# Kernel tuning notes

Measured on AMD Instinct MI355X. Metric: run time of the kernel, lower is better.

## Reference

```python
import math
import jax, jax.numpy as jnp
import numpy as np

B, S, D = 4, 2048, 1280
H, HD = 16, 80  # num_heads, head_dim
LOG2E = 1.442695041


def setup_inputs() -> dict:
    key = jax.random.key(0)
    ks = jax.random.split(key, 6)
    hidden_states = jax.random.normal(ks[0], (B, S, D), dtype=jnp.float32)
    # additive causal mask: 0 on/below diagonal, large negative above
    causal = jnp.tril(jnp.ones((S, S), dtype=bool))
    attention_mask = jnp.where(causal, 0.0, -1e9).astype(jnp.float32)[None, None, :, :]
    attention_mask = jnp.broadcast_to(attention_mask, (B, 1, S, S))
    scaling = jax.random.normal(ks[1], (HD,), dtype=jnp.float32)
    fan = 1.0 / math.sqrt(D)
    qkv_w = jax.random.normal(ks[2], (3 * H * HD, D), dtype=jnp.float32) * fan
    qkv_b = jax.random.normal(ks[3], (3 * H * HD,), dtype=jnp.float32) * fan
    o_w = jax.random.normal(ks[4], (D, H * HD), dtype=jnp.float32) * (1.0 / math.sqrt(H * HD))
    o_b = jax.random.normal(ks[5], (D,), dtype=jnp.float32) * fan
    return {
        "hidden_states": hidden_states,
        "attention_mask": attention_mask,
        "scaling": scaling,
        "qkv_w": qkv_w,
        "qkv_b": qkv_b,
        "o_w": o_w,
        "o_b": o_b,
    }


def reference(hidden_states, attention_mask, scaling, qkv_w, qkv_b, o_w, o_b):
    b, s, _ = hidden_states.shape
    qkv = hidden_states @ qkv_w.T + qkv_b  # [b, s, 3*H*HD]
    xq, xk, xv = jnp.split(qkv, [H * HD, 2 * H * HD], axis=-1)
    xq = xq.reshape(b, s, H, HD)
    xk = xk.reshape(b, s, H, HD)
    xv = xv.reshape(b, s, H, HD)
    # per-dim query scaling: softplus(scaling) * log2(e) / sqrt(head_dim)
    scale = jax.nn.softplus(scaling) * (LOG2E / math.sqrt(HD))
    xq = xq * scale[None, None, None, :]
    scores = jnp.einsum("bqhd,bkhd->bhqk", xq, xk) + attention_mask  # [b,H,s,s]
    probs = jax.nn.softmax(scores.astype(jnp.float32), axis=-1).astype(xq.dtype)
    out = jnp.einsum("bhqk,bkhd->bqhd", probs, xv).reshape(b, s, H * HD)
    return out @ o_w.T + o_b
```

## Files before the change

### kernel.cpp

```cpp
#include <hip/hip_runtime.h>
#include <math.h>

#define B_ 4
#define S_ 2048
#define D_ 1280
#define H_ 16
#define HD_ 80
#define HHD (H_ * HD_)
#define QKVN (3 * H_ * HD_)

typedef __bf16 bf16x8 __attribute__((ext_vector_type(8)));
typedef float  f32x4  __attribute__((ext_vector_type(4)));

__global__ __launch_bounds__(256) void cvt_bf16(
    const float* __restrict__ in, __bf16* __restrict__ out, int n8)
{
    const int i = blockIdx.x * 256 + threadIdx.x;
    if (i < n8) {
        const float4 a = ((const float4*)in)[2 * (size_t)i];
        const float4 b = ((const float4*)in)[2 * (size_t)i + 1];
        bf16x8 v = {(__bf16)a.x, (__bf16)a.y, (__bf16)a.z, (__bf16)a.w,
                    (__bf16)b.x, (__bf16)b.y, (__bf16)b.z, (__bf16)b.w};
        *(bf16x8*)(out + 8 * (size_t)i) = v;
    }
}

__device__ __forceinline__ void async_copy16(const void* g, void* l)
{
    __builtin_amdgcn_global_load_lds(
        (const __attribute__((address_space(1))) unsigned int*)g,
        (__attribute__((address_space(3))) unsigned int*)l, 16, 0, 0);
}

__device__ __forceinline__ void stage128x64(
    const __bf16* __restrict__ src, int K, char* lds, int tid)
{
    const int wave = tid >> 6, lane = tid & 63;
#pragma unroll
    for (int i = 0; i < 4; ++i) {
        const int c = (wave * 4 + i) * 64 + lane;
        const int r = c >> 3;
        const int g = (c & 7) ^ (r & 7);
        async_copy16(src + (size_t)r * K + g * 8, lds + (wave * 4 + i) * 1024);
    }
}

__device__ __forceinline__ bf16x8 frag_ld(const char* lds, int m, int j)
{
    return *(const bf16x8*)(lds + m * 128 + ((j ^ (m & 7)) << 4));
}

__device__ __forceinline__ void mfma_loop(
    const __bf16* __restrict__ A, const __bf16* __restrict__ W, int K,
    char* ldsA, char* ldsB, int tid, f32x4 acc[4][4])
{
    const int wave = tid >> 6;
    const int wm = wave >> 1, wn = wave & 1;
    const int l16 = tid & 15, quad = (tid & 63) >> 4;

#pragma unroll
    for (int mi = 0; mi < 4; ++mi)
#pragma unroll
        for (int ni = 0; ni < 4; ++ni) acc[mi][ni] = (f32x4){0.f, 0.f, 0.f, 0.f};

    for (int k0 = 0; k0 < K; k0 += 64) {
        __syncthreads();
        stage128x64(A + k0, K, ldsA, tid);
        stage128x64(W + k0, K, ldsB, tid);
        __syncthreads();
#pragma unroll
        for (int ks = 0; ks < 2; ++ks) {
            bf16x8 af[4], bfr[4];
#pragma unroll
            for (int mi = 0; mi < 4; ++mi)
                af[mi] = frag_ld(ldsA, wm * 64 + mi * 16 + l16, ks * 4 + quad);
#pragma unroll
            for (int ni = 0; ni < 4; ++ni)
                bfr[ni] = frag_ld(ldsB, wn * 64 + ni * 16 + l16, ks * 4 + quad);
#pragma unroll
            for (int mi = 0; mi < 4; ++mi)
#pragma unroll
                for (int ni = 0; ni < 4; ++ni)
                    acc[mi][ni] = __builtin_amdgcn_mfma_f32_16x16x32_bf16(
                        af[mi], bfr[ni], acc[mi][ni], 0, 0, 0);
        }
    }
}

__global__ __launch_bounds__(256) void gemm_qkv_mfma(
    const __bf16* __restrict__ Ab, const __bf16* __restrict__ Wb,
    const float* __restrict__ bias, const float* __restrict__ scaling,
    __bf16* __restrict__ Qb, __bf16* __restrict__ Kb, __bf16* __restrict__ Vtb)
{
    __shared__ __align__(16) char ldsA[128 * 128];
    __shared__ __align__(16) char ldsB[128 * 128];
    const int tid = threadIdx.x;
    const int m0 = blockIdx.y * 128, n0 = blockIdx.x * 128;

    f32x4 acc[4][4];
    mfma_loop(Ab + (size_t)m0 * D_, Wb + (size_t)n0 * D_, D_, ldsA, ldsB, tid, acc);

    const int wave = tid >> 6, wm = wave >> 1, wn = wave & 1;
    const int l16 = tid & 15, quad = (tid & 63) >> 4;
    const int sec = n0 / HHD;

#pragma unroll
    for (int ni = 0; ni < 4; ++ni) {
        const int col = n0 + wn * 64 + ni * 16 + l16;
        const int cis = col - sec * HHD;
        const int h = cis / HD_;
        const int d = cis - h * HD_;
        const float bv = bias[col];
        float qsv = 0.f;
        if (sec == 0)
            qsv = log1pf(expf(scaling[d])) * (1.442695041f / 8.944271910f);
#pragma unroll
        for (int mi = 0; mi < 4; ++mi) {
#pragma unroll
            for (int r = 0; r < 4; ++r) {
                const int row = m0 + wm * 64 + mi * 16 + quad * 4 + r;
                const int bb = row >> 11;
                const int s = row & (S_ - 1);
                const size_t bh = (size_t)(bb * H_ + h);
                const float v = acc[mi][ni][r] + bv;
                if (sec == 0)      Qb[(bh * S_ + s) * HD_ + d] = (__bf16)(v * qsv);
                else if (sec == 1) Kb[(bh * S_ + s) * HD_ + d] = (__bf16)v;
                else               Vtb[(bh * HD_ + d) * S_ + s] = (__bf16)v;
            }
        }
    }
}

__global__ __launch_bounds__(256) void gemm_o_mfma(
    const __bf16* __restrict__ Ab, const __bf16* __restrict__ Wb,
    const float* __restrict__ bias, float* __restrict__ C)
{
    __shared__ __align__(16) char ldsA[128 * 128];
    __shared__ __align__(16) char ldsB[128 * 128];
    const int tid = threadIdx.x;
    const int m0 = blockIdx.y * 128, n0 = blockIdx.x * 128;

    f32x4 acc[4][4];
    mfma_loop(Ab + (size_t)m0 * D_, Wb + (size_t)n0 * D_, D_, ldsA, ldsB, tid, acc);

    const int wave = tid >> 6, wm = wave >> 1, wn = wave & 1;
    const int l16 = tid & 15, quad = (tid & 63) >> 4;

#pragma unroll
    for (int ni = 0; ni < 4; ++ni) {
        const int col = n0 + wn * 64 + ni * 16 + l16;
        const float bv = bias[col];
#pragma unroll
        for (int mi = 0; mi < 4; ++mi) {
#pragma unroll
            for (int r = 0; r < 4; ++r) {
                const int row = m0 + wm * 64 + mi * 16 + quad * 4 + r;
                C[(size_t)row * D_ + col] = acc[mi][ni][r] + bv;
            }
        }
    }
}

template<int CTRL>
__device__ __forceinline__ float dppmov(float v)
{
    return __builtin_bit_cast(float,
        __builtin_amdgcn_update_dpp(0, __builtin_bit_cast(int, v),
                                    CTRL, 0xf, 0xf, true));
}
__device__ __forceinline__ float rmax16(float v)
{
    v = fmaxf(v, dppmov<0xB1>(v));
    v = fmaxf(v, dppmov<0x4E>(v));
    v = fmaxf(v, dppmov<0x141>(v));
    v = fmaxf(v, dppmov<0x140>(v));
    return v;
}
__device__ __forceinline__ float rsum16(float v)
{
    v += dppmov<0xB1>(v);
    v += dppmov<0x4E>(v);
    v += dppmov<0x141>(v);
    v += dppmov<0x140>(v);
    return v;
}

__global__ __launch_bounds__(256, 4) void attn_v5(
    const __bf16* __restrict__ Qb, const __bf16* __restrict__ Kb,
    const __bf16* __restrict__ Vtb, __bf16* __restrict__ out)
{
    __shared__ __align__(16) __bf16 Ps[4][2][16][40];

    const int tid = threadIdx.x;
    const int wave = tid >> 6;
    const int lane = tid & 63;
    const int l16 = lane & 15;
    const int quad = lane >> 4;
    const int b = blockIdx.z, h = blockIdx.y;
    const int bh = b * H_ + h;
    const int x = blockIdx.x;
    const int q_lo = 64 * x + 16 * wave;
    const int q_hi = 64 * (31 - x) + 16 * wave;

    const __bf16* Kbase = Kb + (size_t)bh * S_ * HD_;
    const __bf16* Vbase = Vtb + (size_t)bh * HD_ * S_;

    bf16x8 qfL[3], qfH[3];
    {
        const __bf16* QrowL = Qb + ((size_t)bh * S_ + q_lo + l16) * HD_;
        const __bf16* QrowH = Qb + ((size_t)bh * S_ + q_hi + l16) * HD_;
        qfL[0] = *(const bf16x8*)(QrowL + quad * 8);
        qfL[1] = *(const bf16x8*)(QrowL + 32 + quad * 8);
        qfH[0] = *(const bf16x8*)(QrowH + quad * 8);
        qfH[1] = *(const bf16x8*)(QrowH + 32 + quad * 8);
        bf16x8 zL = {}, zH = {};
        if (quad < 2) {
            zL = *(const bf16x8*)(QrowL + 64 + quad * 8);
            zH = *(const bf16x8*)(QrowH + 64 + quad * 8);
        }
        qfL[2] = zL; qfH[2] = zH;
    }

    float mL[4], lL[4], mH[4], lH[4];
#pragma unroll
    for (int i = 0; i < 4; ++i) { mL[i] = -1e30f; lL[i] = 0.f; mH[i] = -1e30f; lH[i] = 0.f; }
    f32x4 oL[5], oH[5];
#pragma unroll
    for (int t = 0; t < 5; ++t) { oL[t] = (f32x4){0.f,0.f,0.f,0.f}; oH[t] = (f32x4){0.f,0.f,0.f,0.f}; }

    const int nkt_lo = (q_lo + 16 + 31) >> 5;
    const int nkt_hi = (q_hi + 16 + 31) >> 5;

    for (int kt = 0; kt < nkt_hi; ++kt) {
        const int k0 = kt * 32;
        const bool do_lo = (kt < nkt_lo);

        f32x4 sL[2], sH[2];
#pragma unroll
        for (int t = 0; t < 2; ++t) {
            const __bf16* Krow = Kbase + (size_t)(k0 + t * 16 + l16) * HD_;
            const bf16x8 kf0 = *(const bf16x8*)(Krow + quad * 8);
            const bf16x8 kf1 = *(const bf16x8*)(Krow + 32 + quad * 8);
            bf16x8 kf2 = {};
            if (quad < 2) kf2 = *(const bf16x8*)(Krow + 64 + quad * 8);

            f32x4 a = (f32x4){0.f,0.f,0.f,0.f};
            a = __builtin_amdgcn_mfma_f32_16x16x32_bf16(qfH[0], kf0, a, 0, 0, 0);
            a = __builtin_amdgcn_mfma_f32_16x16x32_bf16(qfH[1], kf1, a, 0, 0, 0);
            a = __builtin_amdgcn_mfma_f32_16x16x32_bf16(qfH[2], kf2, a, 0, 0, 0);
            sH[t] = a;
            if (do_lo) {
                f32x4 c = (f32x4){0.f,0.f,0.f,0.f};
                c = __builtin_amdgcn_mfma_f32_16x16x32_bf16(qfL[0], kf0, c, 0, 0, 0);
                c = __builtin_amdgcn_mfma_f32_16x16x32_bf16(qfL[1], kf1, c, 0, 0, 0);
                c = __builtin_amdgcn_mfma_f32_16x16x32_bf16(qfL[2], kf2, c, 0, 0, 0);
                sL[t] = c;
            }
        }

        const int col0 = k0 + l16;

        float aH[4];
        {
            const int row_abs = q_hi + quad * 4;
            float mx[4];
#pragma unroll
            for (int i = 0; i < 4; ++i) {
                float s0 = (col0      <= row_abs + i) ? sH[0][i] : -1e30f;
                float s1 = (col0 + 16 <= row_abs + i) ? sH[1][i] : -1e30f;
                sH[0][i] = s0; sH[1][i] = s1;
                mx[i] = rmax16(fmaxf(s0, s1));
            }
#pragma unroll
            for (int i = 0; i < 4; ++i) {
                const float mn = fmaxf(mH[i], mx[i]);
                aH[i] = __expf(mH[i] - mn);
                mH[i] = mn;
                const float p0 = __expf(sH[0][i] - mn);
                const float p1 = __expf(sH[1][i] - mn);
                sH[0][i] = p0; sH[1][i] = p1;
                lH[i] = lH[i] * aH[i] + rsum16(p0 + p1);
            }
#pragma unroll
            for (int i = 0; i < 4; ++i) {
                Ps[wave][0][quad * 4 + i][l16]      = (__bf16)sH[0][i];
                Ps[wave][0][quad * 4 + i][16 + l16] = (__bf16)sH[1][i];
            }
        }

        float aL[4];
        if (do_lo) {
            const int row_abs = q_lo + quad * 4;
            float mx[4];
#pragma unroll
            for (int i = 0; i < 4; ++i) {
                float s0 = (col0      <= row_abs + i) ? sL[0][i] : -1e30f;
                float s1 = (col0 + 16 <= row_abs + i) ? sL[1][i] : -1e30f;
                sL[0][i] = s0; sL[1][i] = s1;
                mx[i] = rmax16(fmaxf(s0, s1));
            }
#pragma unroll
            for (int i = 0; i < 4; ++i) {
                const float mn = fmaxf(mL[i], mx[i]);
                aL[i] = __expf(mL[i] - mn);
                mL[i] = mn;
                const float p0 = __expf(sL[0][i] - mn);
                const float p1 = __expf(sL[1][i] - mn);
                sL[0][i] = p0; sL[1][i] = p1;
                lL[i] = lL[i] * aL[i] + rsum16(p0 + p1);
            }
#pragma unroll
            for (int i = 0; i < 4; ++i) {
                Ps[wave][1][quad * 4 + i][l16]      = (__bf16)sL[0][i];
                Ps[wave][1][quad * 4 + i][16 + l16] = (__bf16)sL[1][i];
            }
        }

        asm volatile("s_waitcnt lgkmcnt(0)" ::: "memory");
        const bf16x8 pfH = *(const bf16x8*)&Ps[wave][0][l16][quad * 8];
        const bf16x8 pfL = *(const bf16x8*)&Ps[wave][1][l16][quad * 8];

#pragma unroll
        for (int t = 0; t < 5; ++t) {
            const bf16x8 vf = *(const bf16x8*)(Vbase + (size_t)(t * 16 + l16) * S_ + k0 + quad * 8);
            f32x4 c;
#pragma unroll
            for (int i = 0; i < 4; ++i) c[i] = oH[t][i] * aH[i];
            oH[t] = __builtin_amdgcn_mfma_f32_16x16x32_bf16(pfH, vf, c, 0, 0, 0);
            if (do_lo) {
                f32x4 d;
#pragma unroll
                for (int i = 0; i < 4; ++i) d[i] = oL[t][i] * aL[i];
                oL[t] = __builtin_amdgcn_mfma_f32_16x16x32_bf16(pfL, vf, d, 0, 0, 0);
            }
        }
    }

#pragma unroll
    for (int i = 0; i < 4; ++i) {
        const float invH = 1.f / lH[i];
        const float invL = 1.f / lL[i];
        const size_t rowH = ((size_t)b * S_ + q_hi + quad * 4 + i) * HHD + h * HD_;
        const size_t rowL = ((size_t)b * S_ + q_lo + quad * 4 + i) * HHD + h * HD_;
#pragma unroll
        for (int t = 0; t < 5; ++t) {
            out[rowH + t * 16 + l16] = (__bf16)(oH[t][i] * invH);
            out[rowL + t * 16 + l16] = (__bf16)(oL[t][i] * invL);
        }
    }
}

extern "C" void kernel_launch(void* const* d_in, const int* in_sizes, int n_in,
                              void* d_out, int out_size, void* d_ws, size_t ws_size,
                              hipStream_t stream)
{
    const float* hidden  = (const float*)d_in[0];
    const float* scaling = (const float*)d_in[2];
    const float* qkv_w   = (const float*)d_in[3];
    const float* qkv_b   = (const float*)d_in[4];
    const float* o_w     = (const float*)d_in[5];
    const float* o_b     = (const float*)d_in[6];
    float* out = (float*)d_out;

    const size_t N_HID = (size_t)B_ * S_ * D_;
    const size_t N_QW  = (size_t)QKVN * D_;
    const size_t N_OW  = (size_t)D_ * D_;
    const size_t NPH   = (size_t)B_ * H_ * S_ * HD_;

    __bf16* Ab    = (__bf16*)d_ws;
    __bf16* Wqb   = Ab + N_HID;
    __bf16* Wob   = Wqb + N_QW;
    __bf16* Qb    = Wob + N_OW;
    __bf16* Kb    = Qb + NPH;
    __bf16* Vtb   = Kb + NPH;
    __bf16* attnb = Vtb + NPH;

    dim3 blk(256);

    cvt_bf16<<<dim3(N_HID / 8 / 256), blk, 0, stream>>>(hidden, Ab, N_HID / 8);
    cvt_bf16<<<dim3(N_QW  / 8 / 256), blk, 0, stream>>>(qkv_w, Wqb, N_QW / 8);
    cvt_bf16<<<dim3(N_OW  / 8 / 256), blk, 0, stream>>>(o_w,   Wob, N_OW / 8);

    gemm_qkv_mfma<<<dim3(QKVN / 128, B_ * S_ / 128), blk, 0, stream>>>(
        Ab, Wqb, qkv_b, scaling, Qb, Kb, Vtb);

    attn_v5<<<dim3(16, H_, B_), blk, 0, stream>>>(Qb, Kb, Vtb, attnb);

    gemm_o_mfma<<<dim3(D_ / 128, B_ * S_ / 128), blk, 0, stream>>>(
        attnb, Wob, o_b, out);
}
```

Baseline: 547.2 us.

## Widen attention key tile to 64, skip mask on full tiles, use exp2

```diff
diff --git a/kernel.cpp b/kernel.cpp
--- a/kernel.cpp
+++ b/kernel.cpp
@@ -113,7 +113,8 @@
         const float bv = bias[col];
         float qsv = 0.f;
         if (sec == 0)
-            qsv = log1pf(expf(scaling[d])) * (1.442695041f / 8.944271910f);
+            qsv = log1pf(expf(scaling[d])) *
+                  (1.442695041f * 1.442695041f / 8.944271910f);
 #pragma unroll
         for (int mi = 0; mi < 4; ++mi) {
 #pragma unroll
@@ -185,11 +186,11 @@
     return v;
 }
 
-__global__ __launch_bounds__(256, 4) void attn_v5(
+__global__ __launch_bounds__(256, 4) void attn_v6(
     const __bf16* __restrict__ Qb, const __bf16* __restrict__ Kb,
     const __bf16* __restrict__ Vtb, __bf16* __restrict__ out)
 {
-    __shared__ __align__(16) __bf16 Ps[4][2][16][40];
+    __shared__ __align__(16) __bf16 Ps[4][2][16][72];
 
     const int tid = threadIdx.x;
     const int wave = tid >> 6;
@@ -228,16 +229,16 @@
 #pragma unroll
     for (int t = 0; t < 5; ++t) { oL[t] = (f32x4){0.f,0.f,0.f,0.f}; oH[t] = (f32x4){0.f,0.f,0.f,0.f}; }
 
-    const int nkt_lo = (q_lo + 16 + 31) >> 5;
-    const int nkt_hi = (q_hi + 16 + 31) >> 5;
+    const int nkt_lo = (q_lo + 16 + 63) >> 6;
+    const int nkt_hi = (q_hi + 16 + 63) >> 6;
 
     for (int kt = 0; kt < nkt_hi; ++kt) {
-        const int k0 = kt * 32;
+        const int k0 = kt * 64;
         const bool do_lo = (kt < nkt_lo);
 
-        f32x4 sL[2], sH[2];
-#pragma unroll
-        for (int t = 0; t < 2; ++t) {
+        f32x4 sH[4], sL[4];
+#pragma unroll
+        for (int t = 0; t < 4; ++t) {
             const __bf16* Krow = Kbase + (size_t)(k0 + t * 16 + l16) * HD_;
             const bf16x8 kf0 = *(const bf16x8*)(Krow + quad * 8);
             const bf16x8 kf1 = *(const bf16x8*)(Krow + 32 + quad * 8);
@@ -258,80 +259,96 @@
             }
         }
 
-        const int col0 = k0 + l16;
-
         float aH[4];
         {
-            const int row_abs = q_hi + quad * 4;
-            float mx[4];
-#pragma unroll
-            for (int i = 0; i < 4; ++i) {
-                float s0 = (col0      <= row_abs + i) ? sH[0][i] : -1e30f;
-                float s1 = (col0 + 16 <= row_abs + i) ? sH[1][i] : -1e30f;
-                sH[0][i] = s0; sH[1][i] = s1;
-                mx[i] = rmax16(fmaxf(s0, s1));
-            }
+            if (k0 + 63 > q_hi) {
+#pragma unroll
+                for (int t = 0; t < 4; ++t)
+#pragma unroll
+                    for (int i = 0; i < 4; ++i)
+                        sH[t][i] = (k0 + t * 16 + l16 <= q_hi + quad * 4 + i)
+                                   ? sH[t][i] : -1e30f;
+            }
+            float mx[4], rs[4];
+#pragma unroll
+            for (int i = 0; i < 4; ++i)
+                mx[i] = rmax16(fmaxf(fmaxf(sH[0][i], sH[1][i]),
+                                     fmaxf(sH[2][i], sH[3][i])));
 #pragma unroll
             for (int i = 0; i < 4; ++i) {
                 const float mn = fmaxf(mH[i], mx[i]);
-                aH[i] = __expf(mH[i] - mn);
+                aH[i] = exp2f(mH[i] - mn);
                 mH[i] = mn;
-                const float p0 = __expf(sH[0][i] - mn);
-                const float p1 = __expf(sH[1][i] - mn);
-                sH[0][i] = p0; sH[1][i] = p1;
-                lH[i] = lH[i] * aH[i] + rsum16(p0 + p1);
-            }
-#pragma unroll
-            for (int i = 0; i < 4; ++i) {
-                Ps[wave][0][quad * 4 + i][l16]      = (__bf16)sH[0][i];
-                Ps[wave][0][quad * 4 + i][16 + l16] = (__bf16)sH[1][i];
-            }
+                rs[i] = 0.f;
+            }
+#pragma unroll
+            for (int t = 0; t < 4; ++t)
+#pragma unroll
+                for (int i = 0; i < 4; ++i) {
+                    const float p = exp2f(sH[t][i] - mH[i]);
+                    rs[i] += p;
+                    Ps[wave][0][quad * 4 + i][t * 16 + l16] = (__bf16)p;
+                }
+#pragma unroll
+            for (int i = 0; i < 4; ++i) lH[i] = lH[i] * aH[i] + rsum16(rs[i]);
         }
 
         float aL[4];
         if (do_lo) {
-            const int row_abs = q_lo + quad * 4;
-            float mx[4];
-#pragma unroll
-            for (int i = 0; i < 4; ++i) {
-                float s0 = (col0      <= row_abs + i) ? sL[0][i] : -1e30f;
-                float s1 = (col0 + 16 <= row_abs + i) ? sL[1][i] : -1e30f;
-                sL[0][i] = s0; sL[1][i] = s1;
-                mx[i] = rmax16(fmaxf(s0, s1));
-            }
+            if (k0 + 63 > q_lo) {
+#pragma unroll
+                for (int t = 0; t < 4; ++t)
+#pragma unroll
+                    for (int i = 0; i < 4; ++i)
+                        sL[t][i] = (k0 + t * 16 + l16 <= q_lo + quad * 4 + i)
+                                   ? sL[t][i] : -1e30f;
+            }
+            float mx[4], rs[4];
+#pragma unroll
+            for (int i = 0; i < 4; ++i)
+                mx[i] = rmax16(fmaxf(fmaxf(sL[0][i], sL[1][i]),
+                                     fmaxf(sL[2][i], sL[3][i])));
 #pragma unroll
             for (int i = 0; i < 4; ++i) {
                 const float mn = fmaxf(mL[i], mx[i]);
-                aL[i] = __expf(mL[i] - mn);
+                aL[i] = exp2f(mL[i] - mn);
                 mL[i] = mn;
-                const float p0 = __expf(sL[0][i] - mn);
-                const float p1 = __expf(sL[1][i] - mn);
-                sL[0][i] = p0; sL[1][i] = p1;
-                lL[i] = lL[i] * aL[i] + rsum16(p0 + p1);
-            }
-#pragma unroll
-            for (int i = 0; i < 4; ++i) {
-                Ps[wave][1][quad * 4 + i][l16]      = (__bf16)sL[0][i];
-                Ps[wave][1][quad * 4 + i][16 + l16] = (__bf16)sL[1][i];
-            }
+                rs[i] = 0.f;
+            }
+#pragma unroll
+            for (int t = 0; t < 4; ++t)
+#pragma unroll
+                for (int i = 0; i < 4; ++i) {
+                    const float p = exp2f(sL[t][i] - mL[i]);
+                    rs[i] += p;
+                    Ps[wave][1][quad * 4 + i][t * 16 + l16] = (__bf16)p;
+                }
+#pragma unroll
+            for (int i = 0; i < 4; ++i) lL[i] = lL[i] * aL[i] + rsum16(rs[i]);
         }
 
         asm volatile("s_waitcnt lgkmcnt(0)" ::: "memory");
-        const bf16x8 pfH = *(const bf16x8*)&Ps[wave][0][l16][quad * 8];
-        const bf16x8 pfL = *(const bf16x8*)&Ps[wave][1][l16][quad * 8];
+        const bf16x8 pfH0 = *(const bf16x8*)&Ps[wave][0][l16][quad * 8];
+        const bf16x8 pfH1 = *(const bf16x8*)&Ps[wave][0][l16][32 + quad * 8];
+        const bf16x8 pfL0 = *(const bf16x8*)&Ps[wave][1][l16][quad * 8];
+        const bf16x8 pfL1 = *(const bf16x8*)&Ps[wave][1][l16][32 + quad * 8];
 
 #pragma unroll
         for (int t = 0; t < 5; ++t) {
-            const bf16x8 vf = *(const bf16x8*)(Vbase + (size_t)(t * 16 + l16) * S_ + k0 + quad * 8);
+            const __bf16* Vrow = Vbase + (size_t)(t * 16 + l16) * S_ + k0;
+            const bf16x8 vf0 = *(const bf16x8*)(Vrow + quad * 8);
+            const bf16x8 vf1 = *(const bf16x8*)(Vrow + 32 + quad * 8);
             f32x4 c;
 #pragma unroll
             for (int i = 0; i < 4; ++i) c[i] = oH[t][i] * aH[i];
-            oH[t] = __builtin_amdgcn_mfma_f32_16x16x32_bf16(pfH, vf, c, 0, 0, 0);
+            c = __builtin_amdgcn_mfma_f32_16x16x32_bf16(pfH0, vf0, c, 0, 0, 0);
+            oH[t] = __builtin_amdgcn_mfma_f32_16x16x32_bf16(pfH1, vf1, c, 0, 0, 0);
             if (do_lo) {
                 f32x4 d;
 #pragma unroll
                 for (int i = 0; i < 4; ++i) d[i] = oL[t][i] * aL[i];
-                oL[t] = __builtin_amdgcn_mfma_f32_16x16x32_bf16(pfL, vf, d, 0, 0, 0);
+                d = __builtin_amdgcn_mfma_f32_16x16x32_bf16(pfL0, vf0, d, 0, 0, 0);
+                oL[t] = __builtin_amdgcn_mfma_f32_16x16x32_bf16(pfL1, vf1, d, 0, 0, 0);
             }
         }
     }
@@ -384,7 +401,7 @@
     gemm_qkv_mfma<<<dim3(QKVN / 128, B_ * S_ / 128), blk, 0, stream>>>(
         Ab, Wqb, qkv_b, scaling, Qb, Kb, Vtb);
 
-    attn_v5<<<dim3(16, H_, B_), blk, 0, stream>>>(Qb, Kb, Vtb, attnb);
+    attn_v6<<<dim3(16, H_, B_), blk, 0, stream>>>(Qb, Kb, Vtb, attnb);
 
     gemm_o_mfma<<<dim3(D_ / 128, B_ * S_ / 128), blk, 0, stream>>>(
         attnb, Wob, o_b, out);
```

Measured after the change: 577.3 us. 5.5% more time.

## Transpose attention MFMA operands so each lane owns one query row

Applied to the files above, without the earlier changes.

```diff
diff --git a/kernel.cpp b/kernel.cpp
--- a/kernel.cpp
+++ b/kernel.cpp
@@ -10,6 +10,7 @@
 #define QKVN (3 * H_ * HD_)
 
 typedef __bf16 bf16x8 __attribute__((ext_vector_type(8)));
+typedef __bf16 bf16x4 __attribute__((ext_vector_type(4)));
 typedef float  f32x4  __attribute__((ext_vector_type(4)));
 
 __global__ __launch_bounds__(256) void cvt_bf16(
@@ -113,7 +114,8 @@
         const float bv = bias[col];
         float qsv = 0.f;
         if (sec == 0)
-            qsv = log1pf(expf(scaling[d])) * (1.442695041f / 8.944271910f);
+            qsv = log1pf(expf(scaling[d])) *
+                  (1.442695041f * 1.442695041f / 8.944271910f);
 #pragma unroll
         for (int mi = 0; mi < 4; ++mi) {
 #pragma unroll
@@ -161,31 +163,7 @@
     }
 }
 
-template<int CTRL>
-__device__ __forceinline__ float dppmov(float v)
-{
-    return __builtin_bit_cast(float,
-        __builtin_amdgcn_update_dpp(0, __builtin_bit_cast(int, v),
-                                    CTRL, 0xf, 0xf, true));
-}
-__device__ __forceinline__ float rmax16(float v)
-{
-    v = fmaxf(v, dppmov<0xB1>(v));
-    v = fmaxf(v, dppmov<0x4E>(v));
-    v = fmaxf(v, dppmov<0x141>(v));
-    v = fmaxf(v, dppmov<0x140>(v));
-    return v;
-}
-__device__ __forceinline__ float rsum16(float v)
-{
-    v += dppmov<0xB1>(v);
-    v += dppmov<0x4E>(v);
-    v += dppmov<0x141>(v);
-    v += dppmov<0x140>(v);
-    return v;
-}
-
-__global__ __launch_bounds__(256, 4) void attn_v5(
+__global__ __launch_bounds__(256, 4) void attn_v7(
     const __bf16* __restrict__ Qb, const __bf16* __restrict__ Kb,
     const __bf16* __restrict__ Vtb, __bf16* __restrict__ out)
 {
@@ -221,9 +199,7 @@
         qfL[2] = zL; qfH[2] = zH;
     }
 
-    float mL[4], lL[4], mH[4], lH[4];
-#pragma unroll
-    for (int i = 0; i < 4; ++i) { mL[i] = -1e30f; lL[i] = 0.f; mH[i] = -1e30f; lH[i] = 0.f; }
+    float mL = -1e30f, lL = 0.f, mH = -1e30f, lH = 0.f;
     f32x4 oL[5], oH[5];
 #pragma unroll
     for (int t = 0; t < 5; ++t) { oL[t] = (f32x4){0.f,0.f,0.f,0.f}; oH[t] = (f32x4){0.f,0.f,0.f,0.f}; }
@@ -235,7 +211,7 @@
         const int k0 = kt * 32;
         const bool do_lo = (kt < nkt_lo);
 
-        f32x4 sL[2], sH[2];
+        f32x4 sH[2], sL[2];
 #pragma unroll
         for (int t = 0; t < 2; ++t) {
             const __bf16* Krow = Kbase + (size_t)(k0 + t * 16 + l16) * HD_;
@@ -245,76 +221,103 @@
             if (quad < 2) kf2 = *(const bf16x8*)(Krow + 64 + quad * 8);
 
             f32x4 a = (f32x4){0.f,0.f,0.f,0.f};
-            a = __builtin_amdgcn_mfma_f32_16x16x32_bf16(qfH[0], kf0, a, 0, 0, 0);
-            a = __builtin_amdgcn_mfma_f32_16x16x32_bf16(qfH[1], kf1, a, 0, 0, 0);
-            a = __builtin_amdgcn_mfma_f32_16x16x32_bf16(qfH[2], kf2, a, 0, 0, 0);
+            a = __builtin_amdgcn_mfma_f32_16x16x32_bf16(kf0, qfH[0], a, 0, 0, 0);
+            a = __builtin_amdgcn_mfma_f32_16x16x32_bf16(kf1, qfH[1], a, 0, 0, 0);
+            a = __builtin_amdgcn_mfma_f32_16x16x32_bf16(kf2, qfH[2], a, 0, 0, 0);
             sH[t] = a;
             if (do_lo) {
                 f32x4 c = (f32x4){0.f,0.f,0.f,0.f};
-                c = __builtin_amdgcn_mfma_f32_16x16x32_bf16(qfL[0], kf0, c, 0, 0, 0);
-                c = __builtin_amdgcn_mfma_f32_16x16x32_bf16(qfL[1], kf1, c, 0, 0, 0);
-                c = __builtin_amdgcn_mfma_f32_16x16x32_bf16(qfL[2], kf2, c, 0, 0, 0);
+                c = __builtin_amdgcn_mfma_f32_16x16x32_bf16(kf0, qfL[0], c, 0, 0, 0);
+                c = __builtin_amdgcn_mfma_f32_16x16x32_bf16(kf1, qfL[1], c, 0, 0, 0);
+                c = __builtin_amdgcn_mfma_f32_16x16x32_bf16(kf2, qfL[2], c, 0, 0, 0);
                 sL[t] = c;
             }
         }
 
-        const int col0 = k0 + l16;
-
-        float aH[4];
+        float aH;
         {
-            const int row_abs = q_hi + quad * 4;
-            float mx[4];
-#pragma unroll
-            for (int i = 0; i < 4; ++i) {
-                float s0 = (col0      <= row_abs + i) ? sH[0][i] : -1e30f;
-                float s1 = (col0 + 16 <= row_abs + i) ? sH[1][i] : -1e30f;
-                sH[0][i] = s0; sH[1][i] = s1;
-                mx[i] = rmax16(fmaxf(s0, s1));
-            }
-#pragma unroll
-            for (int i = 0; i < 4; ++i) {
-                const float mn = fmaxf(mH[i], mx[i]);
-                aH[i] = __expf(mH[i] - mn);
-                mH[i] = mn;
-                const float p0 = __expf(sH[0][i] - mn);
-                const float p1 = __expf(sH[1][i] - mn);
-                sH[0][i] = p0; sH[1][i] = p1;
-                lH[i] = lH[i] * aH[i] + rsum16(p0 + p1);
-            }
-#pragma unroll
-            for (int i = 0; i < 4; ++i) {
-                Ps[wave][0][quad * 4 + i][l16]      = (__bf16)sH[0][i];
-                Ps[wave][0][quad * 4 + i][16 + l16] = (__bf16)sH[1][i];
-            }
-        }
-
-        float aL[4];
+            if (k0 + 31 > q_hi) {
+#pragma unroll
+                for (int t = 0; t < 2; ++t)
+#pragma unroll
+                    for (int i = 0; i < 4; ++i)
+                        sH[t][i] = (k0 + t * 16 + quad * 4 + i <= q_hi + l16)
+                                   ? sH[t][i] : -1e30f;
+            }
+            float mx = sH[0][0];
+#pragma unroll
+            for (int i = 1; i < 4; ++i) mx = fmaxf(mx, sH[0][i]);
+#pragma unroll
+            for (int i = 0; i < 4; ++i) mx = fmaxf(mx, sH[1][i]);
+            mx = fmaxf(mx, __shfl_xor(mx, 16));
+            mx = fmaxf(mx, __shfl_xor(mx, 32));
+            const float mn = fmaxf(mH, mx);
+            aH = exp2f(mH - mn);
+            mH = mn;
+            float rs = 0.f;
+#pragma unroll
+            for (int t = 0; t < 2; ++t)
+#pragma unroll
+                for (int i = 0; i < 4; ++i) {
+                    const float p = exp2f(sH[t][i] - mn);
+                    sH[t][i] = p;
+                    rs += p;
+                }
+            rs += __shfl_xor(rs, 16);
+            rs += __shfl_xor(rs, 32);
+            lH = lH * aH + rs;
+#pragma unroll
+            for (int t = 0; t < 2; ++t) {
+                bf16x4 pk = {(__bf16)sH[t][0], (__bf16)sH[t][1],
+                             (__bf16)sH[t][2], (__bf16)sH[t][3]};
+                *(bf16x4*)&Ps[wave][0][l16][t * 16 + quad * 4] = pk;
+            }
+        }
+
+        float aL = 1.f;
         if (do_lo) {
-            const int row_abs = q_lo + quad * 4;
-            float mx[4];
-#pragma unroll
-            for (int i = 0; i < 4; ++i) {
-                float s0 = (col0      <= row_abs + i) ? sL[0][i] : -1e30f;
-                float s1 = (col0 + 16 <= row_abs + i) ? sL[1][i] : -1e30f;
-                sL[0][i] = s0; sL[1][i] = s1;
-                mx[i] = rmax16(fmaxf(s0, s1));
-            }
-#pragma unroll
-            for (int i = 0; i < 4; ++i) {
-                const float mn = fmaxf(mL[i], mx[i]);
-                aL[i] = __expf(mL[i] - mn);
-                mL[i] = mn;
-                const float p0 = __expf(sL[0][i] - mn);
-                const float p1 = __expf(sL[1][i] - mn);
-                sL[0][i] = p0; sL[1][i] = p1;
-                lL[i] = lL[i] * aL[i] + rsum16(p0 + p1);
-            }
-#pragma unroll
-            for (int i = 0; i < 4; ++i) {
-                Ps[wave][1][quad * 4 + i][l16]      = (__bf16)sL[0][i];
-                Ps[wave][1][quad * 4 + i][16 + l16] = (__bf16)sL[1][i];
-            }
-        }
+            if (k0 + 31 > q_lo) {
+#pragma unroll
+                for (int t = 0; t < 2; ++t)
+#pragma unroll
+                    for (int i = 0; i < 4; ++i)
+                        sL[t][i] = (k0 + t * 16 + quad * 4 + i <= q_lo + l16)
+                                   ? sL[t][i] : -1e30f;
+            }
+            float mx = sL[0][0];
+#pragma unroll
+            for (int i = 1; i < 4; ++i) mx = fmaxf(mx, sL[0][i]);
+#pragma unroll
+            for (int i = 0; i < 4; ++i) mx = fmaxf(mx, sL[1][i]);
+            mx = fmaxf(mx, __shfl_xor(mx, 16));
+            mx = fmaxf(mx, __shfl_xor(mx, 32));
+            const float mn = fmaxf(mL, mx);
+            aL = exp2f(mL - mn);
+            mL = mn;
+            float rs = 0.f;
+#pragma unroll
+            for (int t = 0; t < 2; ++t)
+#pragma unroll
+                for (int i = 0; i < 4; ++i) {
+                    const float p = exp2f(sL[t][i] - mn);
+                    sL[t][i] = p;
+                    rs += p;
+                }
+            rs += __shfl_xor(rs, 16);
+            rs += __shfl_xor(rs, 32);
+            lL = lL * aL + rs;
+#pragma unroll
+            for (int t = 0; t < 2; ++t) {
+                bf16x4 pk = {(__bf16)sL[t][0], (__bf16)sL[t][1],
+                             (__bf16)sL[t][2], (__bf16)sL[t][3]};
+                *(bf16x4*)&Ps[wave][1][l16][t * 16 + quad * 4] = pk;
+            }
+        }
+
+        bf16x8 vf[5];
+#pragma unroll
+        for (int t = 0; t < 5; ++t)
+            vf[t] = *(const bf16x8*)(Vbase + (size_t)(t * 16 + l16) * S_ + k0 + quad * 8);
 
         asm volatile("s_waitcnt lgkmcnt(0)" ::: "memory");
         const bf16x8 pfH = *(const bf16x8*)&Ps[wave][0][l16][quad * 8];
@@ -322,31 +325,31 @@
 
 #pragma unroll
         for (int t = 0; t < 5; ++t) {
-            const bf16x8 vf = *(const bf16x8*)(Vbase + (size_t)(t * 16 + l16) * S_ + k0 + quad * 8);
             f32x4 c;
 #pragma unroll
-            for (int i = 0; i < 4; ++i) c[i] = oH[t][i] * aH[i];
-            oH[t] = __builtin_amdgcn_mfma_f32_16x16x32_bf16(pfH, vf, c, 0, 0, 0);
+            for (int i = 0; i < 4; ++i) c[i] = oH[t][i] * aH;
+            oH[t] = __builtin_amdgcn_mfma_f32_16x16x32_bf16(vf[t], pfH, c, 0, 0, 0);
             if (do_lo) {
                 f32x4 d;
 #pragma unroll
-                for (int i = 0; i < 4; ++i) d[i] = oL[t][i] * aL[i];
-                oL[t] = __builtin_amdgcn_mfma_f32_16x16x32_bf16(pfL, vf, d, 0, 0, 0);
-            }
-        }
-    }
-
-#pragma unroll
-    for (int i = 0; i < 4; ++i) {
-        const float invH = 1.f / lH[i];
-        const float invL = 1.f / lL[i];
-        const size_t rowH = ((size_t)b * S_ + q_hi + quad * 4 + i) * HHD + h * HD_;
-        const size_t rowL = ((size_t)b * S_ + q_lo + quad * 4 + i) * HHD + h * HD_;
-#pragma unroll
-        for (int t = 0; t < 5; ++t) {
-            out[rowH + t * 16 + l16] = (__bf16)(oH[t][i] * invH);
-            out[rowL + t * 16 + l16] = (__bf16)(oL[t][i] * invL);
-        }
+                for (int i = 0; i < 4; ++i) d[i] = oL[t][i] * aL;
+                oL[t] = __builtin_amdgcn_mfma_f32_16x16x32_bf16(vf[t], pfL, d, 0, 0, 0);
+            }
+        }
+    }
+
+    const float invH = 1.f / lH;
+    const float invL = 1.f / lL;
+    const size_t rowH = ((size_t)b * S_ + q_hi + l16) * HHD + h * HD_ + quad * 4;
+    const size_t rowL = ((size_t)b * S_ + q_lo + l16) * HHD + h * HD_ + quad * 4;
+#pragma unroll
+    for (int t = 0; t < 5; ++t) {
+        bf16x4 ovH = {(__bf16)(oH[t][0] * invH), (__bf16)(oH[t][1] * invH),
+                      (__bf16)(oH[t][2] * invH), (__bf16)(oH[t][3] * invH)};
+        bf16x4 ovL = {(__bf16)(oL[t][0] * invL), (__bf16)(oL[t][1] * invL),
+                      (__bf16)(oL[t][2] * invL), (__bf16)(oL[t][3] * invL)};
+        *(bf16x4*)(out + rowH + t * 16) = ovH;
+        *(bf16x4*)(out + rowL + t * 16) = ovL;
     }
 }
 
@@ -384,7 +387,7 @@
     gemm_qkv_mfma<<<dim3(QKVN / 128, B_ * S_ / 128), blk, 0, stream>>>(
         Ab, Wqb, qkv_b, scaling, Qb, Kb, Vtb);
 
-    attn_v5<<<dim3(16, H_, B_), blk, 0, stream>>>(Qb, Kb, Vtb, attnb);
+    attn_v7<<<dim3(16, H_, B_), blk, 0, stream>>>(Qb, Kb, Vtb, attnb);
 
     gemm_o_mfma<<<dim3(D_ / 128, B_ * S_ / 128), blk, 0, stream>>>(
         attnb, Wob, o_b, out);
```

Result: no change. 537.6 us (-1.8%).
